# Kernel tuning notes

Measured on AMD Instinct MI355X. Metric: run time of the kernel, lower is better.

## Reference

```python
import jax, jax.numpy as jnp
import numpy as np

N_NODES = 100000
N_FEAT = 500
N_HID = 16
N_CLS = 7
N_EDGES = 3200000


def setup_inputs() -> dict:
    key = jax.random.key(0)
    k1, k2, k3, k4 = jax.random.split(key, 4)
    x = jax.random.normal(k1, (N_NODES, N_FEAT), dtype=jnp.float32)
    edge_index = jax.random.randint(k2, (2, N_EDGES), 0, N_NODES, dtype=jnp.int32)
    # Glorot-style init for the two GCNConv weight matrices
    W1 = jax.random.normal(k3, (N_FEAT, N_HID), dtype=jnp.float32) * (1.0 / np.sqrt(N_FEAT))
    b1 = jnp.zeros((N_HID,), dtype=jnp.float32)
    W2 = jax.random.normal(k4, (N_HID, N_CLS), dtype=jnp.float32) * (1.0 / np.sqrt(N_HID))
    b2 = jnp.zeros((N_CLS,), dtype=jnp.float32)
    return {"x": x, "edge_index": edge_index, "W1": W1, "b1": b1, "W2": W2, "b2": b2}


def _gcn_norm(edge_index, n_nodes):
    # Add self-loops, compute symmetric normalization D^-1/2 (A+I) D^-1/2
    loop = jnp.arange(n_nodes, dtype=edge_index.dtype)
    src = jnp.concatenate([edge_index[0], loop])  # [E+N]
    dst = jnp.concatenate([edge_index[1], loop])  # [E+N]
    deg = jax.ops.segment_sum(jnp.ones_like(dst, dtype=jnp.float32), dst, num_segments=n_nodes)
    dinv = jnp.where(deg > 0, jax.lax.rsqrt(deg), 0.0)
    norm = dinv[src] * dinv[dst]  # [E+N]
    return src, dst, norm


def _gcn_conv(h, W, b, src, dst, norm, n_nodes):
    m = h @ W                                   # [N, out] dense projection first (small out dim)
    agg = jax.ops.segment_sum(m[src] * norm[:, None], dst, num_segments=n_nodes)
    return agg + b


def reference(x, edge_index, W1, b1, W2, b2):
    n = x.shape[0]
    src, dst, norm = _gcn_norm(edge_index, n)
    h = jax.nn.relu(_gcn_conv(x, W1, b1, src, dst, norm, n))
    # dropout is identity in eval mode (training=False)
    logits = _gcn_conv(h, W2, b2, src, dst, norm, n)
    return jax.nn.log_softmax(logits, axis=1)
```

## Files before the change

### kernel.cpp

```cpp
#include <hip/hip_runtime.h>
#include <math.h>

#define N_NODES 100000
#define N_EDGES 3200000
#define N_FEAT  500
#define NF4     125
#define N_HID   16
#define N_CLS   7

#define BKT_SHIFT 7
#define BKT_SIZE  128
#define NBKT      782
#define NBLK_BIN  256
#define EDGES_PER_BLK 12500
#define COUNTS_LEN (NBKT * NBLK_BIN)
#define NBLK_SCANA (COUNTS_LEN / 256)
#define SBUF_CAP  5632

#define OFF_DINV   0
#define OFF_COUNTS 100000
#define OFF_BSUM   300192
#define OFF_ROWP   301216
#define OFF_BINNED 401220
#define OFF_SORTED 3601220
#define OFF_WP     6801220
#define OFF_M1S    6809412
#define OFF_M2S    7609412

typedef __attribute__((ext_vector_type(8))) short short8v;
typedef __attribute__((ext_vector_type(4))) float f32x4v;

__device__ inline unsigned short f2bf(float f) {
    unsigned int u = __float_as_uint(f);
    return (unsigned short)((u + 0x7FFF + ((u >> 16) & 1)) >> 16);
}
__device__ inline float bf2f(unsigned short h) {
    return __uint_as_float((unsigned int)h << 16);
}

__global__ void hist(const int* __restrict__ dst, int* __restrict__ counts) {
    __shared__ int cnt[NBKT];
    int t = threadIdx.x, b = blockIdx.x;
    for (int i = t; i < NBKT; i += 256) cnt[i] = 0;
    __syncthreads();
    const int4* d4 = (const int4*)(dst + b * EDGES_PER_BLK);
    for (int k = t; k < EDGES_PER_BLK / 4; k += 256) {
        int4 d = d4[k];
        atomicAdd(&cnt[d.x >> BKT_SHIFT], 1);
        atomicAdd(&cnt[d.y >> BKT_SHIFT], 1);
        atomicAdd(&cnt[d.z >> BKT_SHIFT], 1);
        atomicAdd(&cnt[d.w >> BKT_SHIFT], 1);
    }
    __syncthreads();
    for (int i = t; i < NBKT; i += 256)
        counts[i * NBLK_BIN + b] = cnt[i];
}

__global__ void scanA(int* __restrict__ counts, int* __restrict__ bsum) {
    __shared__ int s[256];
    int t = threadIdx.x;
    int i = blockIdx.x * 256 + t;
    int v = counts[i];
    s[t] = v;
    __syncthreads();
    for (int off = 1; off < 256; off <<= 1) {
        int a = (t >= off) ? s[t - off] : 0;
        __syncthreads();
        s[t] += a;
        __syncthreads();
    }
    counts[i] = s[t] - v;
    if (t == 255) bsum[blockIdx.x] = s[255];
}

__global__ void scanB(int* __restrict__ bsum) {
    __shared__ int s[1024];
    int t = threadIdx.x;
    int v = (t < NBLK_SCANA) ? bsum[t] : 0;
    s[t] = v;
    __syncthreads();
    for (int off = 1; off < 1024; off <<= 1) {
        int a = (t >= off) ? s[t - off] : 0;
        __syncthreads();
        s[t] += a;
        __syncthreads();
    }
    if (t < NBLK_SCANA) bsum[t] = s[t] - v;
}

__global__ void binpass(const int* __restrict__ src, const int* __restrict__ dst,
                        const int* __restrict__ counts, const int* __restrict__ bsum,
                        unsigned int* __restrict__ binned) {
    __shared__ int cur[NBKT];
    int t = threadIdx.x, b = blockIdx.x;
    for (int i = t; i < NBKT; i += 256) cur[i] = counts[i * NBLK_BIN + b] + bsum[i];
    __syncthreads();
    const int4* s4 = (const int4*)(src + b * EDGES_PER_BLK);
    const int4* d4 = (const int4*)(dst + b * EDGES_PER_BLK);
    for (int k = t; k < EDGES_PER_BLK / 4; k += 256) {
        int4 d = d4[k];
        int4 s = s4[k];
        int pos;
        pos = atomicAdd(&cur[d.x >> BKT_SHIFT], 1);
        binned[pos] = (unsigned int)s.x | ((unsigned int)(d.x & (BKT_SIZE - 1)) << 17);
        pos = atomicAdd(&cur[d.y >> BKT_SHIFT], 1);
        binned[pos] = (unsigned int)s.y | ((unsigned int)(d.y & (BKT_SIZE - 1)) << 17);
        pos = atomicAdd(&cur[d.z >> BKT_SHIFT], 1);
        binned[pos] = (unsigned int)s.z | ((unsigned int)(d.z & (BKT_SIZE - 1)) << 17);
        pos = atomicAdd(&cur[d.w >> BKT_SHIFT], 1);
        binned[pos] = (unsigned int)s.w | ((unsigned int)(d.w & (BKT_SIZE - 1)) << 17);
    }
}

__global__ __launch_bounds__(512) void sortA(const unsigned int* __restrict__ binned,
        const int* __restrict__ counts, const int* __restrict__ bsum,
        int* __restrict__ rowptr, float* __restrict__ dinv) {
    __shared__ int cnt[BKT_SIZE];
    __shared__ int sc[BKT_SIZE];
    int t = threadIdx.x, b = blockIdx.x;
    int beg = counts[b * NBLK_BIN] + bsum[b];
    int end = (b < NBKT - 1) ? counts[(b + 1) * NBLK_BIN] + bsum[b + 1] : N_EDGES;
    if (t < BKT_SIZE) cnt[t] = 0;
    __syncthreads();
    for (int e = beg + t; e < end; e += 512)
        atomicAdd(&cnt[(binned[e] >> 17) & (BKT_SIZE - 1)], 1);
    __syncthreads();
    int v = (t < BKT_SIZE) ? cnt[t] : 0;
    if (t < BKT_SIZE) sc[t] = v;
    __syncthreads();
    for (int off = 1; off < BKT_SIZE; off <<= 1) {
        int a = (t < BKT_SIZE && t >= off) ? sc[t - off] : 0;
        __syncthreads();
        if (t < BKT_SIZE) sc[t] += a;
        __syncthreads();
    }
    if (t < BKT_SIZE) {
        int g = b * BKT_SIZE + t;
        if (g < N_NODES) {
            rowptr[g] = beg + sc[t] - v;
            dinv[g] = rsqrtf((float)v + 1.0f);
        }
    }
    if (b == 0 && t == 0) rowptr[N_NODES] = N_EDGES;
}

__global__ void wpack(const float* __restrict__ W1, uint4* __restrict__ wp) {
    int p = blockIdx.x * 256 + threadIdx.x;
    if (p >= 1024) return;
    int s = p >> 6, l = p & 63;
    int col = l & 15, kb = s * 32 + (l >> 4) * 8;
    unsigned int hw[4], lw[4];
#pragma unroll
    for (int d = 0; d < 4; ++d) {
        unsigned int hpair = 0, lpair = 0;
#pragma unroll
        for (int e = 0; e < 2; ++e) {
            int k = kb + d * 2 + e;
            float w0 = (k < N_FEAT) ? W1[k * 16 + col] : 0.f;
            unsigned int u = __float_as_uint(w0);
            unsigned int uh = u & 0xFFFF0000u;
            float res = w0 - __uint_as_float(uh);
            hpair |= (uh >> 16) << (16 * e);
            lpair |= (unsigned int)f2bf(res) << (16 * e);
        }
        hw[d] = hpair; lw[d] = lpair;
    }
    wp[p] = make_uint4(hw[0], hw[1], hw[2], hw[3]);
    wp[1024 + p] = make_uint4(lw[0], lw[1], lw[2], lw[3]);
}

#define G1_NBLK 1563

__device__ inline void split8(const float4 a, const float4 b, short8v& hi, short8v& lo) {
    float f[8] = {a.x, a.y, a.z, a.w, b.x, b.y, b.z, b.w};
#pragma unroll
    for (int i = 0; i < 8; ++i) {
        unsigned int u = __float_as_uint(f[i]);
        unsigned int uh = u & 0xFFFF0000u;
        hi[i] = (short)(u >> 16);
        lo[i] = (short)f2bf(f[i] - __uint_as_float(uh));
    }
}

__global__ __launch_bounds__(256) void gemm1(const float* __restrict__ x,
        const uint4* __restrict__ wp, const float* __restrict__ dinv,
        unsigned short* __restrict__ m1s) {
    __shared__ uint4 swp[2048];
    const int t = threadIdx.x, b = blockIdx.x;
    const int lane = t & 63, w = t >> 6;
#pragma unroll
    for (int i = 0; i < 8; ++i) swp[i * 256 + t] = wp[i * 256 + t];
    __syncthreads();

    const int r16 = lane & 15, g = lane >> 4;
    const int rowbase = b * 64 + w * 16;
    const int row = rowbase + r16;
    const int srow = (row < N_NODES) ? row : 0;
    const float* pA = x + (size_t)srow * N_FEAT + g * 8;
    const float* t0 = (g <= 2) ? pA + 480 : x;
    const float* t1 = (g <= 1) ? pA + 484 : x;

    float4 a0_0 = *(const float4*)(pA);       float4 a1_0 = *(const float4*)(pA + 4);
    float4 a0_1 = *(const float4*)(pA + 32);  float4 a1_1 = *(const float4*)(pA + 36);
    float4 a0_2 = *(const float4*)(pA + 64);  float4 a1_2 = *(const float4*)(pA + 68);

    f32x4v acc = {0.f, 0.f, 0.f, 0.f};
#pragma unroll
    for (int s = 0; s < 16; ++s) {
        float4 xa, xb;
        if ((s % 3) == 0)      { xa = a0_0; xb = a1_0; }
        else if ((s % 3) == 1) { xa = a0_1; xb = a1_1; }
        else                   { xa = a0_2; xb = a1_2; }
        short8v ah, al;
        split8(xa, xb, ah, al);
        if (s < 13) {
            const float* p = (s == 12) ? t0 : pA + (s + 3) * 32;
            const float* q = (s == 12) ? t1 : pA + (s + 3) * 32 + 4;
            float4 n0 = *(const float4*)p;
            float4 n1 = *(const float4*)q;
            if ((s % 3) == 0)      { a0_0 = n0; a1_0 = n1; }
            else if ((s % 3) == 1) { a0_1 = n0; a1_1 = n1; }
            else                   { a0_2 = n0; a1_2 = n1; }
        }
        short8v bh = *reinterpret_cast<const short8v*>(&swp[s * 64 + lane]);
        short8v bl = *reinterpret_cast<const short8v*>(&swp[1024 + s * 64 + lane]);
        acc = __builtin_amdgcn_mfma_f32_16x16x32_bf16(ah, bh, acc, 0, 0, 0);
        acc = __builtin_amdgcn_mfma_f32_16x16x32_bf16(al, bh, acc, 0, 0, 0);
        acc = __builtin_amdgcn_mfma_f32_16x16x32_bf16(ah, bl, acc, 0, 0, 0);
    }

#pragma unroll
    for (int j = 0; j < 4; ++j) {
        int r = rowbase + g * 4 + j;
        if (r < N_NODES) m1s[(size_t)r * 16 + r16] = f2bf(acc[j] * dinv[r]);
    }
}

__global__ __launch_bounds__(512) void sortAgg1(const unsigned int* __restrict__ binned,
        const int* __restrict__ counts, const int* __restrict__ bsum,
        const int* __restrict__ rowptr, const float* __restrict__ dinv,
        const unsigned short* __restrict__ m1s, const float* __restrict__ b1,
        const float* __restrict__ W2, unsigned int* __restrict__ sorted,
        unsigned short* __restrict__ m2s) {
    __shared__ unsigned int sbuf[SBUF_CAP];
    __shared__ int cur[BKT_SIZE];
    __shared__ float acc[BKT_SIZE * 17];
    __shared__ float sW2[N_HID * N_CLS];
    __shared__ float sb1[N_HID];
    int t = threadIdx.x, b = blockIdx.x;
    if (t < N_HID * N_CLS) sW2[t] = W2[t];
    if (t < N_HID) sb1[t] = b1[t];
    int beg = counts[b * NBLK_BIN] + bsum[b];
    int end = (b < NBKT - 1) ? counts[(b + 1) * NBLK_BIN] + bsum[b + 1] : N_EDGES;
    if (t < BKT_SIZE) {
        int g = b * BKT_SIZE + t;
        cur[t] = ((g < N_NODES) ? rowptr[g] : end) - beg;
    }
    __syncthreads();
    for (int e = beg + t; e < end; e += 512) {
        unsigned int u = binned[e];
        int pos = atomicAdd(&cur[(u >> 17) & (BKT_SIZE - 1)], 1);
        if (pos < SBUF_CAP) sbuf[pos] = u & 0x1FFFF;
    }
    __syncthreads();
    int n = end - beg;
    for (int i = t; i < n; i += 512) sorted[beg + i] = sbuf[i];
    {
        int nn = t >> 2, q = t & 3;
        int g = b * BKT_SIZE + nn;
        float a0 = 0.f, a1 = 0.f, a2 = 0.f, a3 = 0.f;
        if (g < N_NODES) {
            int lbeg = rowptr[g] - beg;
            int lend = ((g + 1 <= N_NODES) ? rowptr[g + 1] : N_EDGES) - beg;
            int p = lbeg;
            for (; p + 1 < lend; p += 2) {
                unsigned int s0 = sbuf[p], s1 = sbuf[p + 1];
                uint2 w0 = *(const uint2*)&m1s[(size_t)s0 * 16 + q * 4];
                uint2 w1 = *(const uint2*)&m1s[(size_t)s1 * 16 + q * 4];
                a0 += __uint_as_float(w0.x << 16);
                a1 += __uint_as_float(w0.x & 0xFFFF0000u);
                a2 += __uint_as_float(w0.y << 16);
                a3 += __uint_as_float(w0.y & 0xFFFF0000u);
                a0 += __uint_as_float(w1.x << 16);
                a1 += __uint_as_float(w1.x & 0xFFFF0000u);
                a2 += __uint_as_float(w1.y << 16);
                a3 += __uint_as_float(w1.y & 0xFFFF0000u);
            }
            if (p < lend) {
                unsigned int s0 = sbuf[p];
                uint2 w0 = *(const uint2*)&m1s[(size_t)s0 * 16 + q * 4];
                a0 += __uint_as_float(w0.x << 16);
                a1 += __uint_as_float(w0.x & 0xFFFF0000u);
                a2 += __uint_as_float(w0.y << 16);
                a3 += __uint_as_float(w0.y & 0xFFFF0000u);
            }
        }
        __syncthreads();
        float* ap = &acc[nn * 17 + q * 4];
        ap[0] = a0; ap[1] = a1; ap[2] = a2; ap[3] = a3;
    }
    __syncthreads();
    for (int idx = t; idx < BKT_SIZE * 16; idx += 512) {
        int nn = idx >> 4, jj = idx & 15;
        int gg = b * BKT_SIZE + nn;
        if (gg < N_NODES) {
            float di = dinv[gg];
            float hv = di * (acc[nn * 17 + jj] + bf2f(m1s[(size_t)gg * 16 + jj])) + sb1[jj];
            acc[nn * 17 + jj] = hv > 0.f ? hv : 0.f;
        }
    }
    __syncthreads();
    for (int idx = t; idx < BKT_SIZE * 8; idx += 512) {
        int nn = idx >> 3, cc = idx & 7;
        int gg = b * BKT_SIZE + nn;
        if (gg < N_NODES) {
            float sum = 0.f;
            if (cc < N_CLS) {
#pragma unroll
                for (int jj = 0; jj < N_HID; ++jj) sum += acc[nn * 17 + jj] * sW2[jj * 7 + cc];
                sum *= dinv[gg];
            }
            m2s[(size_t)gg * 8 + cc] = f2bf(sum);
        }
    }
}

__global__ __launch_bounds__(256) void agg2(const unsigned int* __restrict__ sorted,
        const int* __restrict__ rowptr, const float* __restrict__ dinv,
        const unsigned short* __restrict__ m2s, const float* __restrict__ b2,
        float* __restrict__ out) {
    __shared__ float acc[BKT_SIZE * 9];
    int t = threadIdx.x, b = blockIdx.x;
    int n = t >> 1, q = t & 1;
    int g = b * BKT_SIZE + n;
    float a0 = 0.f, a1 = 0.f, a2 = 0.f, a3 = 0.f;
    if (g < N_NODES) {
        int beg = rowptr[g], end = rowptr[g + 1];
        int p = beg;
        for (; p + 1 < end; p += 2) {
            unsigned int s0 = sorted[p], s1 = sorted[p + 1];
            uint2 w0 = *(const uint2*)&m2s[(size_t)s0 * 8 + q * 4];
            uint2 w1 = *(const uint2*)&m2s[(size_t)s1 * 8 + q * 4];
            a0 += __uint_as_float(w0.x << 16);
            a1 += __uint_as_float(w0.x & 0xFFFF0000u);
            a2 += __uint_as_float(w0.y << 16);
            a3 += __uint_as_float(w0.y & 0xFFFF0000u);
            a0 += __uint_as_float(w1.x << 16);
            a1 += __uint_as_float(w1.x & 0xFFFF0000u);
            a2 += __uint_as_float(w1.y << 16);
            a3 += __uint_as_float(w1.y & 0xFFFF0000u);
        }
        if (p < end) {
            unsigned int s0 = sorted[p];
            uint2 w0 = *(const uint2*)&m2s[(size_t)s0 * 8 + q * 4];
            a0 += __uint_as_float(w0.x << 16);
            a1 += __uint_as_float(w0.x & 0xFFFF0000u);
            a2 += __uint_as_float(w0.y << 16);
            a3 += __uint_as_float(w0.y & 0xFFFF0000u);
        }
    }
    float* ap = &acc[n * 9 + q * 4];
    ap[0] = a0; ap[1] = a1; ap[2] = a2; ap[3] = a3;
    __syncthreads();
    int j = t & 7;
    for (int pass = 0; pass < 4; ++pass) {
        int nn = (t >> 3) + pass * 32;
        int gg = b * BKT_SIZE + nn;
        bool valid = (gg < N_NODES) && (j < N_CLS);
        float v = -1e30f;
        if (valid) {
            float di = dinv[gg];
            v = di * (acc[nn * 9 + j] + bf2f(m2s[(size_t)gg * 8 + j])) + b2[j];
        }
        float mx = v;
#pragma unroll
        for (int off = 1; off < 8; off <<= 1) mx = fmaxf(mx, __shfl_xor(mx, off, 8));
        float ex = valid ? expf(v - mx) : 0.f;
        float sum = ex;
#pragma unroll
        for (int off = 1; off < 8; off <<= 1) sum += __shfl_xor(sum, off, 8);
        float ls = mx + logf(sum);
        if (valid) out[(size_t)gg * 7 + j] = v - ls;
    }
}

extern "C" void kernel_launch(void* const* d_in, const int* in_sizes, int n_in,
                              void* d_out, int out_size, void* d_ws, size_t ws_size,
                              hipStream_t stream) {
    const float* x  = (const float*)d_in[0];
    const int*   ei = (const int*)d_in[1];
    const float* W1 = (const float*)d_in[2];
    const float* b1 = (const float*)d_in[3];
    const float* W2 = (const float*)d_in[4];
    const float* b2 = (const float*)d_in[5];
    float* out = (float*)d_out;
    char*  wsb = (char*)d_ws;

    const int* src = ei;
    const int* dst = ei + N_EDGES;

    float*          dinv   = (float*)wsb + OFF_DINV;
    int*            counts = (int*)wsb + OFF_COUNTS;
    int*            bsum   = (int*)wsb + OFF_BSUM;
    int*            rowptr = (int*)wsb + OFF_ROWP;
    unsigned int*   binned = (unsigned int*)wsb + OFF_BINNED;
    unsigned int*   sorted = (unsigned int*)wsb + OFF_SORTED;
    uint4*          wp     = (uint4*)((int*)wsb + OFF_WP);
    unsigned short* m1s    = (unsigned short*)(wsb + (size_t)OFF_M1S * 4);
    unsigned short* m2s    = (unsigned short*)(wsb + (size_t)OFF_M2S * 4);

    hist     <<<NBLK_BIN, 256, 0, stream>>>(dst, counts);
    scanA    <<<NBLK_SCANA, 256, 0, stream>>>(counts, bsum);
    scanB    <<<1, 1024, 0, stream>>>(bsum);
    binpass  <<<NBLK_BIN, 256, 0, stream>>>(src, dst, counts, bsum, binned);
    sortA    <<<NBKT, 512, 0, stream>>>(binned, counts, bsum, rowptr, dinv);
    wpack    <<<4, 256, 0, stream>>>(W1, wp);
    gemm1    <<<G1_NBLK, 256, 0, stream>>>(x, wp, dinv, m1s);
    sortAgg1 <<<NBKT, 512, 0, stream>>>(binned, counts, bsum, rowptr, dinv,
                                        m1s, b1, W2, sorted, m2s);
    agg2     <<<NBKT, 256, 0, stream>>>(sorted, rowptr, dinv, m2s, b2, out);
}
```

Measured before the change: 438.1 us.

## Fuse wpack into scanB, deepen gemm1 prefetch, unroll gathers, widen agg2

The W1 packing kernel is merged into the single-block scanB launch, which removes one kernel launch. gemm1 now prefetches six K-chunks ahead instead of three, giving more memory-level parallelism at the cost of more registers. The gather loops in sortAgg1 and agg2 are unrolled by four, and agg2 now uses 512 threads with four lanes per node, each doing 4-byte loads, so more loads are in flight per node.

```diff
diff --git a/kernel.cpp b/kernel.cpp
--- a/kernel.cpp
+++ b/kernel.cpp
@@ -73,9 +73,33 @@
     if (t == 255) bsum[blockIdx.x] = s[255];
 }
 
-__global__ void scanB(int* __restrict__ bsum) {
+__global__ void scanB_wpack(int* __restrict__ bsum, const float* __restrict__ W1,
+                            uint4* __restrict__ wp) {
+    int t = threadIdx.x;
+    {
+        int p = t;
+        int s = p >> 6, l = p & 63;
+        int col = l & 15, kb = s * 32 + (l >> 4) * 8;
+        unsigned int hw[4], lw[4];
+#pragma unroll
+        for (int d = 0; d < 4; ++d) {
+            unsigned int hpair = 0, lpair = 0;
+#pragma unroll
+            for (int e = 0; e < 2; ++e) {
+                int k = kb + d * 2 + e;
+                float w0 = (k < N_FEAT) ? W1[k * 16 + col] : 0.f;
+                unsigned int u = __float_as_uint(w0);
+                unsigned int uh = u & 0xFFFF0000u;
+                float res = w0 - __uint_as_float(uh);
+                hpair |= (uh >> 16) << (16 * e);
+                lpair |= (unsigned int)f2bf(res) << (16 * e);
+            }
+            hw[d] = hpair; lw[d] = lpair;
+        }
+        wp[p] = make_uint4(hw[0], hw[1], hw[2], hw[3]);
+        wp[1024 + p] = make_uint4(lw[0], lw[1], lw[2], lw[3]);
+    }
     __shared__ int s[1024];
-    int t = threadIdx.x;
     int v = (t < NBLK_SCANA) ? bsum[t] : 0;
     s[t] = v;
     __syncthreads();
@@ -144,31 +168,6 @@
     if (b == 0 && t == 0) rowptr[N_NODES] = N_EDGES;
 }
 
-__global__ void wpack(const float* __restrict__ W1, uint4* __restrict__ wp) {
-    int p = blockIdx.x * 256 + threadIdx.x;
-    if (p >= 1024) return;
-    int s = p >> 6, l = p & 63;
-    int col = l & 15, kb = s * 32 + (l >> 4) * 8;
-    unsigned int hw[4], lw[4];
-#pragma unroll
-    for (int d = 0; d < 4; ++d) {
-        unsigned int hpair = 0, lpair = 0;
-#pragma unroll
-        for (int e = 0; e < 2; ++e) {
-            int k = kb + d * 2 + e;
-            float w0 = (k < N_FEAT) ? W1[k * 16 + col] : 0.f;
-            unsigned int u = __float_as_uint(w0);
-            unsigned int uh = u & 0xFFFF0000u;
-            float res = w0 - __uint_as_float(uh);
-            hpair |= (uh >> 16) << (16 * e);
-            lpair |= (unsigned int)f2bf(res) << (16 * e);
-        }
-        hw[d] = hpair; lw[d] = lpair;
-    }
-    wp[p] = make_uint4(hw[0], hw[1], hw[2], hw[3]);
-    wp[1024 + p] = make_uint4(lw[0], lw[1], lw[2], lw[3]);
-}
-
 #define G1_NBLK 1563
 
 __device__ inline void split8(const float4 a, const float4 b, short8v& hi, short8v& lo) {
@@ -200,28 +199,42 @@
     const float* t0 = (g <= 2) ? pA + 480 : x;
     const float* t1 = (g <= 1) ? pA + 484 : x;
 
-    float4 a0_0 = *(const float4*)(pA);       float4 a1_0 = *(const float4*)(pA + 4);
-    float4 a0_1 = *(const float4*)(pA + 32);  float4 a1_1 = *(const float4*)(pA + 36);
-    float4 a0_2 = *(const float4*)(pA + 64);  float4 a1_2 = *(const float4*)(pA + 68);
+    float4 a0_0 = *(const float4*)(pA);        float4 a1_0 = *(const float4*)(pA + 4);
+    float4 a0_1 = *(const float4*)(pA + 32);   float4 a1_1 = *(const float4*)(pA + 36);
+    float4 a0_2 = *(const float4*)(pA + 64);   float4 a1_2 = *(const float4*)(pA + 68);
+    float4 a0_3 = *(const float4*)(pA + 96);   float4 a1_3 = *(const float4*)(pA + 100);
+    float4 a0_4 = *(const float4*)(pA + 128);  float4 a1_4 = *(const float4*)(pA + 132);
+    float4 a0_5 = *(const float4*)(pA + 160);  float4 a1_5 = *(const float4*)(pA + 164);
 
     f32x4v acc = {0.f, 0.f, 0.f, 0.f};
 #pragma unroll
     for (int s = 0; s < 16; ++s) {
         float4 xa, xb;
-        if ((s % 3) == 0)      { xa = a0_0; xb = a1_0; }
-        else if ((s % 3) == 1) { xa = a0_1; xb = a1_1; }
-        else                   { xa = a0_2; xb = a1_2; }
+        switch (s % 6) {
+            case 0: xa = a0_0; xb = a1_0; break;
+            case 1: xa = a0_1; xb = a1_1; break;
+            case 2: xa = a0_2; xb = a1_2; break;
+            case 3: xa = a0_3; xb = a1_3; break;
+            case 4: xa = a0_4; xb = a1_4; break;
+            default: xa = a0_5; xb = a1_5; break;
+        }
+        if (s <= 9) {
+            int tg = s + 6;
+            const float* p = (tg == 15) ? t0 : pA + tg * 32;
+            const float* q = (tg == 15) ? t1 : pA + tg * 32 + 4;
+            float4 n0 = *(const float4*)p;
+            float4 n1 = *(const float4*)q;
+            switch (s % 6) {
+                case 0: a0_0 = n0; a1_0 = n1; break;
+                case 1: a0_1 = n0; a1_1 = n1; break;
+                case 2: a0_2 = n0; a1_2 = n1; break;
+                case 3: a0_3 = n0; a1_3 = n1; break;
+                case 4: a0_4 = n0; a1_4 = n1; break;
+                default: a0_5 = n0; a1_5 = n1; break;
+            }
+        }
         short8v ah, al;
         split8(xa, xb, ah, al);
-        if (s < 13) {
-            const float* p = (s == 12) ? t0 : pA + (s + 3) * 32;
-            const float* q = (s == 12) ? t1 : pA + (s + 3) * 32 + 4;
-            float4 n0 = *(const float4*)p;
-            float4 n1 = *(const float4*)q;
-            if ((s % 3) == 0)      { a0_0 = n0; a1_0 = n1; }
-            else if ((s % 3) == 1) { a0_1 = n0; a1_1 = n1; }
-            else                   { a0_2 = n0; a1_2 = n1; }
-        }
         short8v bh = *reinterpret_cast<const short8v*>(&swp[s * 64 + lane]);
         short8v bl = *reinterpret_cast<const short8v*>(&swp[1024 + s * 64 + lane]);
         acc = __builtin_amdgcn_mfma_f32_16x16x32_bf16(ah, bh, acc, 0, 0, 0);
@@ -273,10 +286,13 @@
             int lbeg = rowptr[g] - beg;
             int lend = ((g + 1 <= N_NODES) ? rowptr[g + 1] : N_EDGES) - beg;
             int p = lbeg;
-            for (; p + 1 < lend; p += 2) {
+            for (; p + 3 < lend; p += 4) {
                 unsigned int s0 = sbuf[p], s1 = sbuf[p + 1];
+                unsigned int s2 = sbuf[p + 2], s3 = sbuf[p + 3];
                 uint2 w0 = *(const uint2*)&m1s[(size_t)s0 * 16 + q * 4];
                 uint2 w1 = *(const uint2*)&m1s[(size_t)s1 * 16 + q * 4];
+                uint2 w2 = *(const uint2*)&m1s[(size_t)s2 * 16 + q * 4];
+                uint2 w3 = *(const uint2*)&m1s[(size_t)s3 * 16 + q * 4];
                 a0 += __uint_as_float(w0.x << 16);
                 a1 += __uint_as_float(w0.x & 0xFFFF0000u);
                 a2 += __uint_as_float(w0.y << 16);
@@ -285,8 +301,16 @@
                 a1 += __uint_as_float(w1.x & 0xFFFF0000u);
                 a2 += __uint_as_float(w1.y << 16);
                 a3 += __uint_as_float(w1.y & 0xFFFF0000u);
+                a0 += __uint_as_float(w2.x << 16);
+                a1 += __uint_as_float(w2.x & 0xFFFF0000u);
+                a2 += __uint_as_float(w2.y << 16);
+                a3 += __uint_as_float(w2.y & 0xFFFF0000u);
+                a0 += __uint_as_float(w3.x << 16);
+                a1 += __uint_as_float(w3.x & 0xFFFF0000u);
+                a2 += __uint_as_float(w3.y << 16);
+                a3 += __uint_as_float(w3.y & 0xFFFF0000u);
             }
-            if (p < lend) {
+            for (; p < lend; ++p) {
                 unsigned int s0 = sbuf[p];
                 uint2 w0 = *(const uint2*)&m1s[(size_t)s0 * 16 + q * 4];
                 a0 += __uint_as_float(w0.x << 16);
@@ -325,46 +349,42 @@
     }
 }
 
-__global__ __launch_bounds__(256) void agg2(const unsigned int* __restrict__ sorted,
+__global__ __launch_bounds__(512) void agg2(const unsigned int* __restrict__ sorted,
         const int* __restrict__ rowptr, const float* __restrict__ dinv,
         const unsigned short* __restrict__ m2s, const float* __restrict__ b2,
         float* __restrict__ out) {
     __shared__ float acc[BKT_SIZE * 9];
     int t = threadIdx.x, b = blockIdx.x;
-    int n = t >> 1, q = t & 1;
+    int n = t >> 2, q = t & 3;
     int g = b * BKT_SIZE + n;
-    float a0 = 0.f, a1 = 0.f, a2 = 0.f, a3 = 0.f;
+    float a0 = 0.f, a1 = 0.f;
     if (g < N_NODES) {
         int beg = rowptr[g], end = rowptr[g + 1];
         int p = beg;
-        for (; p + 1 < end; p += 2) {
+        for (; p + 3 < end; p += 4) {
             unsigned int s0 = sorted[p], s1 = sorted[p + 1];
-            uint2 w0 = *(const uint2*)&m2s[(size_t)s0 * 8 + q * 4];
-            uint2 w1 = *(const uint2*)&m2s[(size_t)s1 * 8 + q * 4];
-            a0 += __uint_as_float(w0.x << 16);
-            a1 += __uint_as_float(w0.x & 0xFFFF0000u);
-            a2 += __uint_as_float(w0.y << 16);
-            a3 += __uint_as_float(w0.y & 0xFFFF0000u);
-            a0 += __uint_as_float(w1.x << 16);
-            a1 += __uint_as_float(w1.x & 0xFFFF0000u);
-            a2 += __uint_as_float(w1.y << 16);
-            a3 += __uint_as_float(w1.y & 0xFFFF0000u);
-        }
-        if (p < end) {
+            unsigned int s2 = sorted[p + 2], s3 = sorted[p + 3];
+            unsigned int w0 = *(const unsigned int*)&m2s[(size_t)s0 * 8 + q * 2];
+            unsigned int w1 = *(const unsigned int*)&m2s[(size_t)s1 * 8 + q * 2];
+            unsigned int w2 = *(const unsigned int*)&m2s[(size_t)s2 * 8 + q * 2];
+            unsigned int w3 = *(const unsigned int*)&m2s[(size_t)s3 * 8 + q * 2];
+            a0 += __uint_as_float(w0 << 16); a1 += __uint_as_float(w0 & 0xFFFF0000u);
+            a0 += __uint_as_float(w1 << 16); a1 += __uint_as_float(w1 & 0xFFFF0000u);
+            a0 += __uint_as_float(w2 << 16); a1 += __uint_as_float(w2 & 0xFFFF0000u);
+            a0 += __uint_as_float(w3 << 16); a1 += __uint_as_float(w3 & 0xFFFF0000u);
+        }
+        for (; p < end; ++p) {
             unsigned int s0 = sorted[p];
-            uint2 w0 = *(const uint2*)&m2s[(size_t)s0 * 8 + q * 4];
-            a0 += __uint_as_float(w0.x << 16);
-            a1 += __uint_as_float(w0.x & 0xFFFF0000u);
-            a2 += __uint_as_float(w0.y << 16);
-            a3 += __uint_as_float(w0.y & 0xFFFF0000u);
-        }
-    }
-    float* ap = &acc[n * 9 + q * 4];
-    ap[0] = a0; ap[1] = a1; ap[2] = a2; ap[3] = a3;
+            unsigned int w0 = *(const unsigned int*)&m2s[(size_t)s0 * 8 + q * 2];
+            a0 += __uint_as_float(w0 << 16); a1 += __uint_as_float(w0 & 0xFFFF0000u);
+        }
+    }
+    float* ap = &acc[n * 9 + q * 2];
+    ap[0] = a0; ap[1] = a1;
     __syncthreads();
     int j = t & 7;
-    for (int pass = 0; pass < 4; ++pass) {
-        int nn = (t >> 3) + pass * 32;
+    for (int pass = 0; pass < 2; ++pass) {
+        int nn = (t >> 3) + pass * 64;
         int gg = b * BKT_SIZE + nn;
         bool valid = (gg < N_NODES) && (j < N_CLS);
         float v = -1e30f;
@@ -409,14 +429,13 @@
     unsigned short* m1s    = (unsigned short*)(wsb + (size_t)OFF_M1S * 4);
     unsigned short* m2s    = (unsigned short*)(wsb + (size_t)OFF_M2S * 4);
 
-    hist     <<<NBLK_BIN, 256, 0, stream>>>(dst, counts);
-    scanA    <<<NBLK_SCANA, 256, 0, stream>>>(counts, bsum);
-    scanB    <<<1, 1024, 0, stream>>>(bsum);
-    binpass  <<<NBLK_BIN, 256, 0, stream>>>(src, dst, counts, bsum, binned);
-    sortA    <<<NBKT, 512, 0, stream>>>(binned, counts, bsum, rowptr, dinv);
-    wpack    <<<4, 256, 0, stream>>>(W1, wp);
-    gemm1    <<<G1_NBLK, 256, 0, stream>>>(x, wp, dinv, m1s);
-    sortAgg1 <<<NBKT, 512, 0, stream>>>(binned, counts, bsum, rowptr, dinv,
-                                        m1s, b1, W2, sorted, m2s);
-    agg2     <<<NBKT, 256, 0, stream>>>(sorted, rowptr, dinv, m2s, b2, out);
-}
+    hist       <<<NBLK_BIN, 256, 0, stream>>>(dst, counts);
+    scanA      <<<NBLK_SCANA, 256, 0, stream>>>(counts, bsum);
+    scanB_wpack<<<1, 1024, 0, stream>>>(bsum, W1, wp);
+    binpass    <<<NBLK_BIN, 256, 0, stream>>>(src, dst, counts, bsum, binned);
+    sortA      <<<NBKT, 512, 0, stream>>>(binned, counts, bsum, rowptr, dinv);
+    gemm1      <<<G1_NBLK, 256, 0, stream>>>(x, wp, dinv, m1s);
+    sortAgg1   <<<NBKT, 512, 0, stream>>>(binned, counts, bsum, rowptr, dinv,
+                                          m1s, b1, W2, sorted, m2s);
+    agg2       <<<NBKT, 512, 0, stream>>>(sorted, rowptr, dinv, m2s, b2, out);
+}
```

Measured after the change: 431.7 us. No clear change (-1.5%).
